# Kernel optimization log

Hardware: AMD Instinct MI355X
Metric: run time of the kernel (lower is better)

Reference implementation:

```python
import jax, jax.numpy as jnp
import numpy as np

B, N, E = 4, 8192, 65536
OBS, H, OUT, NOUT = 128, 256, 1024, 18


def setup_inputs() -> dict:
    key = jax.random.key(0)
    ks = jax.random.split(key, 8)
    nodes = jax.random.normal(ks[0], (B, N, OBS), dtype=jnp.float32)
    edges = jax.random.randint(ks[1], (B, 2, E), 0, N, dtype=jnp.int64)
    # Glorot-ish init for weights
    W0 = jax.random.normal(ks[2], (OBS, H), dtype=jnp.float32) / np.float32(np.sqrt(OBS))
    W1 = jax.random.normal(ks[3], (H, OUT), dtype=jnp.float32) / np.float32(np.sqrt(H))
    W_logit = jax.random.normal(ks[4], (OUT, NOUT), dtype=jnp.float32) / np.float32(np.sqrt(OUT))
    W_val = jax.random.normal(ks[5], (OUT, 1), dtype=jnp.float32) / np.float32(np.sqrt(OUT))
    return {
        "nodes": nodes, "edges": edges,
        "W0": W0, "b0": jnp.zeros((H,), jnp.float32),
        "W1": W1, "b1": jnp.zeros((OUT,), jnp.float32),
        "W_logit": W_logit, "b_logit": jnp.zeros((NOUT,), jnp.float32),
        "W_val": W_val, "b_val": jnp.zeros((1,), jnp.float32),
    }


def _gcn_layer(x, src, dst, W, b, n):
    # PyG GCNConv: out = D^{-1/2} (A + I) D^{-1/2} X W + b   (self-loops already in src/dst)
    h = x @ W                                                     # [N, F_out]
    deg = jax.ops.segment_sum(jnp.ones(src.shape, jnp.float32), dst, num_segments=n)
    dinv = jnp.where(deg > 0, jax.lax.rsqrt(deg), 0.0)            # deg^{-1/2}
    norm = dinv[src] * dinv[dst]                                  # [Etot]
    msg = h[src] * norm[:, None]                                  # gather + normalize
    agg = jax.ops.segment_sum(msg, dst, num_segments=n)           # scatter-add
    return agg + b


def reference(nodes, edges, W0, b0, W1, b1, W_logit, b_logit, W_val, b_val):
    n = nodes.shape[1]
    loops = jnp.arange(n, dtype=edges.dtype)  # self-loops, added by GCNConv

    def per_graph(x, ei):
        src = jnp.concatenate([ei[0], loops])
        dst = jnp.concatenate([ei[1], loops])
        h = jax.nn.relu(_gcn_layer(x, src, dst, W0, b0, n))
        # (original applies F.dropout here; omitted for a deterministic reference)
        h = jax.nn.relu(_gcn_layer(h, src, dst, W1, b1, n))
        return h

    out = jax.vmap(per_graph)(nodes, edges)        # [B, N, OUT]
    logits = out @ W_logit + b_logit               # [B, N, NOUT]
    values = (out @ W_val + b_val)[..., 0]         # [B, N]
    return logits, values
```

## Files before the change

kernel.cpp:

```cpp
#include <hip/hip_runtime.h>
#include <hip/hip_bf16.h>

#define BB   4
#define NN   8192
#define EE   65536
#define FOBS 128
#define FH   256
#define FOUT 1024
#define NLOG 18
#define P20  20
#define BKT  64

typedef __attribute__((ext_vector_type(8))) short frag8;
typedef __attribute__((ext_vector_type(4))) float f32x4;

__device__ __forceinline__ ushort f2b(float v) {
    __hip_bfloat16 h = __float2bfloat16(v);
    return *reinterpret_cast<ushort*>(&h);
}
__device__ __forceinline__ float blo(uint u) { return __uint_as_float(u << 16); }
__device__ __forceinline__ float bhi(uint u) { return __uint_as_float(u & 0xffff0000u); }


#define W0_N   (FOBS * FH)
#define W1_N   (FH * FOUT)
#define WH_N   (19 * FOUT)
#define CUR_N  (BB * NN)
#define PREP_TOTAL (W0_N + W1_N + WH_N + CUR_N)

__global__ void prep_kernel(const float* __restrict__ W0, ushort* __restrict__ W0T,
                            const float* __restrict__ W1, ushort* __restrict__ W1T,
                            const float* __restrict__ Wl, const float* __restrict__ Wv,
                            ushort* __restrict__ WT19, int* __restrict__ cursor) {
    int idx = blockIdx.x * blockDim.x + threadIdx.x;
    if (idx < W0_N) {
        int n = idx / FOBS, k = idx - n * FOBS;
        W0T[idx] = f2b(W0[(size_t)k * FH + n]);
        return;
    }
    idx -= W0_N;
    if (idx < W1_N) {
        int n = idx / FH, k = idx - n * FH;
        W1T[idx] = f2b(W1[(size_t)k * FOUT + n]);
        return;
    }
    idx -= W1_N;
    if (idx < WH_N) {
        int o = idx >> 10, k = idx & (FOUT - 1);
        WT19[idx] = f2b((o < NLOG) ? Wl[(size_t)k * NLOG + o] : Wv[k]);
        return;
    }
    idx -= WH_N;
    if (idx < CUR_N) cursor[idx] = 0;
}

__global__ void bucket_fill(const int* __restrict__ edges, int* __restrict__ cursor,
                            int* __restrict__ bucket) {
    int blk = blockIdx.x;
    int xcd = blk & 7;
    int g = xcd >> 1;
    int chunk = (blk >> 3) * 2 + (xcd & 1);
    int e = chunk * 256 + threadIdx.x;
    const int* src = edges + (size_t)g * 2 * EE;
    const int* dst = src + EE;
    int d = dst[e];
    int slot = atomicAdd(&cursor[(size_t)g * NN + d], 1);
    if (slot < BKT) bucket[((size_t)g * NN + d) * BKT + slot] = src[e];
}

__global__ __launch_bounds__(256) void gather_agg_f32(
    const float* __restrict__ x_all, const int* __restrict__ cnt_all,
    const int* __restrict__ bucket, uint* __restrict__ agg_all)
{
    int blk = blockIdx.x;
    int xcd = blk & 7;
    int g = xcd >> 1;
    int local = (blk >> 3) * 2 + (xcd & 1);
    int wv = threadIdx.x >> 6, lane = threadIdx.x & 63;
    int n = local * 4 + wv;

    const float2* x = (const float2*)(x_all + (size_t)g * NN * FOBS);
    const int* cnt = cnt_all + (size_t)g * NN;
    const int* bkt = bucket + ((size_t)g * NN + n) * BKT;

    int cn = cnt[n];
    float wn = rsqrtf((float)cn + 1.0f);
    int deg = min(cn, BKT);

    float2 self = x[(size_t)n * 64 + lane];
    float ax = wn * wn * self.x, ay = wn * wn * self.y;

    for (int i = 0; i < deg; i += 8) {
        int last = deg - 1;
        int s0 = bkt[i];
        int s1 = bkt[min(i + 1, last)], s2 = bkt[min(i + 2, last)], s3 = bkt[min(i + 3, last)];
        int s4 = bkt[min(i + 4, last)], s5 = bkt[min(i + 5, last)], s6 = bkt[min(i + 6, last)];
        int s7 = bkt[min(i + 7, last)];
        float w0 = rsqrtf((float)cnt[s0] + 1.0f) * wn;
        float w1 = (i + 1 < deg) ? rsqrtf((float)cnt[s1] + 1.0f) * wn : 0.0f;
        float w2 = (i + 2 < deg) ? rsqrtf((float)cnt[s2] + 1.0f) * wn : 0.0f;
        float w3 = (i + 3 < deg) ? rsqrtf((float)cnt[s3] + 1.0f) * wn : 0.0f;
        float w4 = (i + 4 < deg) ? rsqrtf((float)cnt[s4] + 1.0f) * wn : 0.0f;
        float w5 = (i + 5 < deg) ? rsqrtf((float)cnt[s5] + 1.0f) * wn : 0.0f;
        float w6 = (i + 6 < deg) ? rsqrtf((float)cnt[s6] + 1.0f) * wn : 0.0f;
        float w7 = (i + 7 < deg) ? rsqrtf((float)cnt[s7] + 1.0f) * wn : 0.0f;
        float2 r0 = x[(size_t)s0 * 64 + lane], r1 = x[(size_t)s1 * 64 + lane];
        float2 r2 = x[(size_t)s2 * 64 + lane], r3 = x[(size_t)s3 * 64 + lane];
        float2 r4 = x[(size_t)s4 * 64 + lane], r5 = x[(size_t)s5 * 64 + lane];
        float2 r6 = x[(size_t)s6 * 64 + lane], r7 = x[(size_t)s7 * 64 + lane];
        ax += w0 * r0.x + w1 * r1.x + w2 * r2.x + w3 * r3.x
            + w4 * r4.x + w5 * r5.x + w6 * r6.x + w7 * r7.x;
        ay += w0 * r0.y + w1 * r1.y + w2 * r2.y + w3 * r3.y
            + w4 * r4.y + w5 * r5.y + w6 * r6.y + w7 * r7.y;
    }
    agg_all[((size_t)g * NN + n) * 64 + lane] = (uint)f2b(ax) | ((uint)f2b(ay) << 16);
}

__global__ __launch_bounds__(256) void gather_agg_b256(
    const uint2* __restrict__ xb_all, const int* __restrict__ cnt_all,
    const int* __restrict__ bucket, uint2* __restrict__ agg_all)
{
    int blk = blockIdx.x;
    int xcd = blk & 7;
    int g = xcd >> 1;
    int local = (blk >> 3) * 2 + (xcd & 1);
    int wv = threadIdx.x >> 6, lane = threadIdx.x & 63;
    int n = local * 4 + wv;

    const uint2* xb = xb_all + (size_t)g * NN * 64;
    const int* cnt = cnt_all + (size_t)g * NN;
    const int* bkt = bucket + ((size_t)g * NN + n) * BKT;

    int cn = cnt[n];
    float wn = rsqrtf((float)cn + 1.0f);
    int deg = min(cn, BKT);

    uint2 u = xb[(size_t)n * 64 + lane];
    float w2s = wn * wn;
    float a0 = w2s * blo(u.x), a1 = w2s * bhi(u.x), a2 = w2s * blo(u.y), a3 = w2s * bhi(u.y);

    for (int i = 0; i < deg; i += 8) {
        int last = deg - 1;
        int s0 = bkt[i];
        int s1 = bkt[min(i + 1, last)], s2 = bkt[min(i + 2, last)], s3 = bkt[min(i + 3, last)];
        int s4 = bkt[min(i + 4, last)], s5 = bkt[min(i + 5, last)], s6 = bkt[min(i + 6, last)];
        int s7 = bkt[min(i + 7, last)];
        float w0 = rsqrtf((float)cnt[s0] + 1.0f) * wn;
        float w1 = (i + 1 < deg) ? rsqrtf((float)cnt[s1] + 1.0f) * wn : 0.0f;
        float w2 = (i + 2 < deg) ? rsqrtf((float)cnt[s2] + 1.0f) * wn : 0.0f;
        float w3 = (i + 3 < deg) ? rsqrtf((float)cnt[s3] + 1.0f) * wn : 0.0f;
        float w4 = (i + 4 < deg) ? rsqrtf((float)cnt[s4] + 1.0f) * wn : 0.0f;
        float w5 = (i + 5 < deg) ? rsqrtf((float)cnt[s5] + 1.0f) * wn : 0.0f;
        float w6 = (i + 6 < deg) ? rsqrtf((float)cnt[s6] + 1.0f) * wn : 0.0f;
        float w7 = (i + 7 < deg) ? rsqrtf((float)cnt[s7] + 1.0f) * wn : 0.0f;
        uint2 r0 = xb[(size_t)s0 * 64 + lane], r1 = xb[(size_t)s1 * 64 + lane];
        uint2 r2 = xb[(size_t)s2 * 64 + lane], r3 = xb[(size_t)s3 * 64 + lane];
        uint2 r4 = xb[(size_t)s4 * 64 + lane], r5 = xb[(size_t)s5 * 64 + lane];
        uint2 r6 = xb[(size_t)s6 * 64 + lane], r7 = xb[(size_t)s7 * 64 + lane];
        a0 += w0 * blo(r0.x) + w1 * blo(r1.x) + w2 * blo(r2.x) + w3 * blo(r3.x)
            + w4 * blo(r4.x) + w5 * blo(r5.x) + w6 * blo(r6.x) + w7 * blo(r7.x);
        a1 += w0 * bhi(r0.x) + w1 * bhi(r1.x) + w2 * bhi(r2.x) + w3 * bhi(r3.x)
            + w4 * bhi(r4.x) + w5 * bhi(r5.x) + w6 * bhi(r6.x) + w7 * bhi(r7.x);
        a2 += w0 * blo(r0.y) + w1 * blo(r1.y) + w2 * blo(r2.y) + w3 * blo(r3.y)
            + w4 * blo(r4.y) + w5 * blo(r5.y) + w6 * blo(r6.y) + w7 * blo(r7.y);
        a3 += w0 * bhi(r0.y) + w1 * bhi(r1.y) + w2 * bhi(r2.y) + w3 * bhi(r3.y)
            + w4 * bhi(r4.y) + w5 * bhi(r5.y) + w6 * bhi(r6.y) + w7 * bhi(r7.y);
    }
    uint2 o;
    o.x = (uint)f2b(a0) | ((uint)f2b(a1) << 16);
    o.y = (uint)f2b(a2) | ((uint)f2b(a3) << 16);
    agg_all[((size_t)g * NN + n) * 64 + lane] = o;
}

__global__ __launch_bounds__(256) void mfma_gemm(
    const ushort* __restrict__ A_all, const ushort* __restrict__ BT,
    const float* __restrict__ bias, ushort* __restrict__ C_all,
    int M, int N, int K, int relu)
{
    __shared__ ushort As[128][72];
    __shared__ ushort Bs[128][72];

    int blk = blockIdx.x;
    int xcd = blk & 7;
    int g = xcd >> 1;
    int tid = (blk >> 3) * 2 + (xcd & 1);
    int bn = tid & 1, bm = tid >> 1;

    const ushort* A = A_all + (size_t)g * M * K;
    ushort* C = C_all + (size_t)g * M * N;

    int t = threadIdx.x;
    int lane = t & 63, w = t >> 6;
    int wm = w >> 1, wn = w & 1;
    int l15 = lane & 15, quad = lane >> 4;

    f32x4 acc[4][4] = {};

    int srow = t >> 3, scol = (t & 7) * 8;
    const ushort* Abase = A + (size_t)(bm * 128) * K;
    const ushort* Bbase = BT + (size_t)(bn * 128) * K;

    for (int k0 = 0; k0 < K; k0 += 64) {
#pragma unroll
        for (int i = 0; i < 4; ++i) {
            int row = srow + 32 * i;
            *(uint4*)&As[row][scol] = *(const uint4*)(Abase + (size_t)row * K + k0 + scol);
        }
#pragma unroll
        for (int i = 0; i < 4; ++i) {
            int row = srow + 32 * i;
            *(uint4*)&Bs[row][scol] = *(const uint4*)(Bbase + (size_t)row * K + k0 + scol);
        }
        __syncthreads();
#pragma unroll
        for (int kk = 0; kk < 64; kk += 32) {
            frag8 af[4], bf[4];
#pragma unroll
            for (int i = 0; i < 4; ++i)
                af[i] = *(const frag8*)&As[wm * 64 + i * 16 + l15][kk + quad * 8];
#pragma unroll
            for (int j = 0; j < 4; ++j)
                bf[j] = *(const frag8*)&Bs[wn * 64 + j * 16 + l15][kk + quad * 8];
#pragma unroll
            for (int i = 0; i < 4; ++i)
#pragma unroll
                for (int j = 0; j < 4; ++j)
                    acc[i][j] = __builtin_amdgcn_mfma_f32_16x16x32_bf16(af[i], bf[j], acc[i][j], 0, 0, 0);
        }
        __syncthreads();
    }

#pragma unroll
    for (int i = 0; i < 4; ++i) {
#pragma unroll
        for (int j = 0; j < 4; ++j) {
            int col = bn * 128 + wn * 64 + j * 16 + l15;
            float bcol = bias[col];
#pragma unroll
            for (int r = 0; r < 4; ++r) {
                int row = bm * 128 + wm * 64 + i * 16 + quad * 4 + r;
                float v = acc[i][j][r] + bcol;
                if (relu) v = fmaxf(v, 0.0f);
                C[(size_t)row * N + col] = f2b(v);
            }
        }
    }
}

__global__ __launch_bounds__(256) void gemm2_heads(
    const ushort* __restrict__ hagg_all,
    const ushort* __restrict__ W1T,
    const float*  __restrict__ b1,
    const ushort* __restrict__ WT19,
    float* __restrict__ partial)
{
    __shared__ __align__(16) ushort smem[2 * 128 * 72];
    __shared__ __align__(16) ushort wt[20][136];

    ushort* As = smem;
    ushort* Bs = smem + 128 * 72;
    ushort* Ct = smem;

    int blk = blockIdx.x;
    int xcd = blk & 7;
    int g = xcd >> 1;
    int tid = (blk >> 3) * 2 + (xcd & 1);
    int sp = tid & 1, bm = tid >> 1;

    int t = threadIdx.x;
    int lane = t & 63, w = t >> 6;
    int wm = w >> 1, wn = w & 1;
    int l15 = lane & 15, quad = lane >> 4;
    int srow = t >> 3, scol = (t & 7) * 8;

    const ushort* A0 = hagg_all + ((size_t)g * NN + bm * 128) * FH;

    if (t < 136) wt[19][t] = 0;

    f32x4 hacc[2][2] = {};

    for (int bi = 0; bi < 4; ++bi) {
        int bn = sp * 4 + bi;
        __syncthreads();

        for (int idx = t; idx < 19 * 16; idx += 256) {
            int row = idx >> 4, c8 = (idx & 15) * 8;
            *(uint4*)&wt[row][c8] = *(const uint4*)(WT19 + (size_t)row * FOUT + bn * 128 + c8);
        }

        f32x4 acc[4][4] = {};
        const ushort* Bbase = W1T + (size_t)(bn * 128) * FH;

        for (int k0 = 0; k0 < FH; k0 += 64) {
#pragma unroll
            for (int i = 0; i < 4; ++i) {
                int row = srow + 32 * i;
                *(uint4*)&As[row * 72 + scol] = *(const uint4*)(A0 + (size_t)row * FH + k0 + scol);
                *(uint4*)&Bs[row * 72 + scol] = *(const uint4*)(Bbase + (size_t)row * FH + k0 + scol);
            }
            __syncthreads();
#pragma unroll
            for (int kk = 0; kk < 64; kk += 32) {
                frag8 af[4], bf[4];
#pragma unroll
                for (int i = 0; i < 4; ++i)
                    af[i] = *(const frag8*)&As[(wm * 64 + i * 16 + l15) * 72 + kk + quad * 8];
#pragma unroll
                for (int j = 0; j < 4; ++j)
                    bf[j] = *(const frag8*)&Bs[(wn * 64 + j * 16 + l15) * 72 + kk + quad * 8];
#pragma unroll
                for (int i = 0; i < 4; ++i)
#pragma unroll
                    for (int j = 0; j < 4; ++j)
                        acc[i][j] = __builtin_amdgcn_mfma_f32_16x16x32_bf16(af[i], bf[j], acc[i][j], 0, 0, 0);
            }
            __syncthreads();
        }

#pragma unroll
        for (int j = 0; j < 4; ++j) {
            int colL = wn * 64 + j * 16 + l15;
            float bcol = b1[bn * 128 + colL];
#pragma unroll
            for (int i = 0; i < 4; ++i) {
                int rowL = wm * 64 + i * 16 + quad * 4;
#pragma unroll
                for (int r = 0; r < 4; ++r) {
                    float v = fmaxf(acc[i][j][r] + bcol, 0.0f);
                    Ct[(size_t)(rowL + r) * 136 + colL] = f2b(v);
                }
            }
        }
        __syncthreads();

        int r1 = (l15 < 3) ? (16 + l15) : 19;
#pragma unroll
        for (int kk = 0; kk < 128; kk += 32) {
            frag8 b0 = *(const frag8*)&wt[l15][kk + quad * 8];
            frag8 bO = *(const frag8*)&wt[r1][kk + quad * 8];
#pragma unroll
            for (int mt = 0; mt < 2; ++mt) {
                int row = (w * 2 + mt) * 16 + l15;
                frag8 af = *(const frag8*)&Ct[(size_t)row * 136 + kk + quad * 8];
                hacc[mt][0] = __builtin_amdgcn_mfma_f32_16x16x32_bf16(af, b0, hacc[mt][0], 0, 0, 0);
                hacc[mt][1] = __builtin_amdgcn_mfma_f32_16x16x32_bf16(af, bO, hacc[mt][1], 0, 0, 0);
            }
        }
    }

#pragma unroll
    for (int mt = 0; mt < 2; ++mt) {
#pragma unroll
        for (int r = 0; r < 4; ++r) {
            int node = bm * 128 + (w * 2 + mt) * 16 + quad * 4 + r;
            size_t base = ((size_t)(sp * BB + g) * NN + node) * P20;
            partial[base + l15] = hacc[mt][0][r];
            if (l15 < 3) partial[base + 16 + l15] = hacc[mt][1][r];
        }
    }
}

__global__ void heads_combine(const float* __restrict__ partial,
                              const float* __restrict__ bl, const float* __restrict__ bv,
                              float* __restrict__ out_logits, float* __restrict__ out_values) {
    int i = blockIdx.x * blockDim.x + threadIdx.x;
    if (i >= BB * NN * 19) return;
    int o = i % 19;
    int gn = i / 19;
    float v = partial[(size_t)gn * P20 + o] + partial[((size_t)BB * NN + gn) * P20 + o];
    if (o < NLOG) out_logits[(size_t)gn * NLOG + o] = v + bl[o];
    else          out_values[gn] = v + bv[0];
}

extern "C" void kernel_launch(void* const* d_in, const int* in_sizes, int n_in,
                              void* d_out, int out_size, void* d_ws, size_t ws_size,
                              hipStream_t stream) {
    const float* nodes = (const float*)d_in[0];
    const int*   edges = (const int*)d_in[1];
    const float* W0 = (const float*)d_in[2];
    const float* b0 = (const float*)d_in[3];
    const float* W1 = (const float*)d_in[4];
    const float* b1 = (const float*)d_in[5];
    const float* Wl = (const float*)d_in[6];
    const float* bl = (const float*)d_in[7];
    const float* Wv = (const float*)d_in[8];
    const float* bv = (const float*)d_in[9];

    float* out_logits = (float*)d_out;
    float* out_values = out_logits + (size_t)BB * NN * NLOG;

    char* ws = (char*)d_ws;
    int*    cursor  = (int*)(ws);
    ushort* W0T     = (ushort*)(ws + (128 << 10));
    ushort* W1T     = (ushort*)(ws + (192 << 10));
    ushort* WT19    = (ushort*)(ws + (704 << 10));
    int*    bucket  = (int*)(ws + (1u << 20));
    ushort* xagg_b  = (ushort*)(ws + (9u << 20));
    ushort* h1b     = (ushort*)(ws + (17u << 20));
    ushort* hagg_b  = (ushort*)(ws + (33u << 20));
    float*  partial = (float*)(ws + (49u << 20));

    prep_kernel<<<(PREP_TOTAL + 255) / 256, 256, 0, stream>>>(
        W0, W0T, W1, W1T, Wl, Wv, WT19, cursor);

    bucket_fill<<<1024, 256, 0, stream>>>(edges, cursor, bucket);

    gather_agg_f32<<<8192, 256, 0, stream>>>(nodes, cursor, bucket, (uint*)xagg_b);

    mfma_gemm<<<512, 256, 0, stream>>>(xagg_b, W0T, b0, h1b, NN, FH, FOBS, 1);

    gather_agg_b256<<<8192, 256, 0, stream>>>((const uint2*)h1b, cursor, bucket,
                                              (uint2*)hagg_b);

    gemm2_heads<<<512, 256, 0, stream>>>(hagg_b, W1T, b1, WT19, partial);

    heads_combine<<<(BB * NN * 19 + 255) / 256, 256, 0, stream>>>(partial, bl, bv,
                                                                  out_logits, out_values);
}
```

Before: 195.7 us.

## Restructure fused GEMM2+heads: full-K resident A tile, double-buffered W1, drop combine kernel

Rewrites the second GEMM fused with the output heads so each block owns a 128-row tile across all 1024 output columns. The full-K A tile stays resident in LDS and W1/head-weight tiles are register-prefetched into a double buffer, so the next tile loads while the current one computes. Because a block no longer splits the column range, the heads accumulate fully in registers and are written directly with biases. This removes the partial buffer and the separate combine kernel. The trade-off is only 256 blocks, each using about 156 KB of dynamic LDS, which lowers occupancy and parallelism on a 256-CU device.

```diff
diff --git a/kernel.cpp b/kernel.cpp
--- a/kernel.cpp
+++ b/kernel.cpp
@@ -8,7 +8,6 @@
 #define FH   256
 #define FOUT 1024
 #define NLOG 18
-#define P20  20
 #define BKT  64
 
 typedef __attribute__((ext_vector_type(8))) short frag8;
@@ -20,7 +19,6 @@
 }
 __device__ __forceinline__ float blo(uint u) { return __uint_as_float(u << 16); }
 __device__ __forceinline__ float bhi(uint u) { return __uint_as_float(u & 0xffff0000u); }
-
 
 #define W0_N   (FOBS * FH)
 #define W1_N   (FH * FOUT)
@@ -247,129 +245,150 @@
     }
 }
 
-__global__ __launch_bounds__(256) void gemm2_heads(
+#define LDS_AS   0
+#define LDS_BS   33792
+#define LDS_BSZ  16896
+#define LDS_CT   67584
+#define LDS_WT   76800
+#define LDS_WTSZ 1440
+#define LDS_SHORTS 79680
+
+__global__ __launch_bounds__(256) void gemm2_heads_v2(
     const ushort* __restrict__ hagg_all,
     const ushort* __restrict__ W1T,
     const float*  __restrict__ b1,
     const ushort* __restrict__ WT19,
-    float* __restrict__ partial)
+    const float* __restrict__ bl, const float* __restrict__ bv,
+    float* __restrict__ out_logits_all, float* __restrict__ out_values_all)
 {
-    __shared__ __align__(16) ushort smem[2 * 128 * 72];
-    __shared__ __align__(16) ushort wt[20][136];
-
-    ushort* As = smem;
-    ushort* Bs = smem + 128 * 72;
-    ushort* Ct = smem;
+    extern __shared__ __align__(16) ushort smem[];
 
     int blk = blockIdx.x;
-    int xcd = blk & 7;
-    int g = xcd >> 1;
-    int tid = (blk >> 3) * 2 + (xcd & 1);
-    int sp = tid & 1, bm = tid >> 1;
-
+    int g = blk & 3, bm = blk >> 2;
     int t = threadIdx.x;
     int lane = t & 63, w = t >> 6;
-    int wm = w >> 1, wn = w & 1;
     int l15 = lane & 15, quad = lane >> 4;
-    int srow = t >> 3, scol = (t & 7) * 8;
 
     const ushort* A0 = hagg_all + ((size_t)g * NN + bm * 128) * FH;
 
-    if (t < 136) wt[19][t] = 0;
+#pragma unroll
+    for (int c = 0; c < 16; ++c) {
+        int idx = c * 256 + t;
+        int row = idx >> 5, c8 = (idx & 31) * 8;
+        *(uint4*)&smem[LDS_AS + row * 264 + c8] = *(const uint4*)(A0 + (size_t)row * FH + c8);
+    }
+#pragma unroll
+    for (int c = 0; c < 8; ++c) {
+        int idx = c * 256 + t;
+        int row = idx >> 5, c8 = (idx & 31) * 8;
+        *(uint4*)&smem[LDS_BS + row * 264 + c8] = *(const uint4*)(W1T + (size_t)row * FH + c8);
+    }
+    if (t < 152) {
+        int row = t >> 3, c8 = (t & 7) * 8;
+        *(uint4*)&smem[LDS_WT + row * 72 + c8] = *(const uint4*)(WT19 + (size_t)row * FOUT + c8);
+    }
+    if (t < 16) {
+        int b = t >> 3, c8 = (t & 7) * 8;
+        uint4 z = {0, 0, 0, 0};
+        *(uint4*)&smem[LDS_WT + b * LDS_WTSZ + 19 * 72 + c8] = z;
+    }
+    __syncthreads();
 
     f32x4 hacc[2][2] = {};
-
-    for (int bi = 0; bi < 4; ++bi) {
-        int bn = sp * 4 + bi;
+    int r1 = (l15 < 3) ? (16 + l15) : 19;
+
+    for (int bn = 0; bn < 16; ++bn) {
+        int cur = bn & 1, nxt = cur ^ 1;
+
+        uint4 pb[8];
+        uint4 pw;
+        if (bn < 15) {
+            const ushort* Bn = W1T + (size_t)(bn + 1) * 64 * FH;
+#pragma unroll
+            for (int c = 0; c < 8; ++c) {
+                int idx = c * 256 + t;
+                int row = idx >> 5, c8 = (idx & 31) * 8;
+                pb[c] = *(const uint4*)(Bn + (size_t)row * FH + c8);
+            }
+            if (t < 152) {
+                int row = t >> 3, c8 = (t & 7) * 8;
+                pw = *(const uint4*)(WT19 + (size_t)row * FOUT + (bn + 1) * 64 + c8);
+            }
+        }
+
+        const ushort* Bb  = &smem[LDS_BS + cur * LDS_BSZ];
+        const ushort* wtb = &smem[LDS_WT + cur * LDS_WTSZ];
+
+        f32x4 acc[2][4] = {};
+#pragma unroll
+        for (int kk = 0; kk < 256; kk += 32) {
+            frag8 af[2], bf[4];
+#pragma unroll
+            for (int mt = 0; mt < 2; ++mt)
+                af[mt] = *(const frag8*)&smem[LDS_AS + (w * 32 + mt * 16 + l15) * 264 + kk + quad * 8];
+#pragma unroll
+            for (int nt = 0; nt < 4; ++nt)
+                bf[nt] = *(const frag8*)&Bb[(nt * 16 + l15) * 264 + kk + quad * 8];
+#pragma unroll
+            for (int mt = 0; mt < 2; ++mt)
+#pragma unroll
+                for (int nt = 0; nt < 4; ++nt)
+                    acc[mt][nt] = __builtin_amdgcn_mfma_f32_16x16x32_bf16(af[mt], bf[nt], acc[mt][nt], 0, 0, 0);
+        }
+
+#pragma unroll
+        for (int nt = 0; nt < 4; ++nt) {
+            float bcol = b1[bn * 64 + nt * 16 + l15];
+#pragma unroll
+            for (int mt = 0; mt < 2; ++mt) {
+                int rbase = w * 32 + mt * 16 + quad * 4;
+#pragma unroll
+                for (int r = 0; r < 4; ++r) {
+                    float v = fmaxf(acc[mt][nt][r] + bcol, 0.0f);
+                    smem[LDS_CT + (rbase + r) * 72 + nt * 16 + l15] = f2b(v);
+                }
+            }
+        }
+
+#pragma unroll
+        for (int kk2 = 0; kk2 < 64; kk2 += 32) {
+            frag8 hb0 = *(const frag8*)&wtb[l15 * 72 + kk2 + quad * 8];
+            frag8 hb1 = *(const frag8*)&wtb[r1 * 72 + kk2 + quad * 8];
+#pragma unroll
+            for (int mt = 0; mt < 2; ++mt) {
+                frag8 haf = *(const frag8*)&smem[LDS_CT + (w * 32 + mt * 16 + l15) * 72 + kk2 + quad * 8];
+                hacc[mt][0] = __builtin_amdgcn_mfma_f32_16x16x32_bf16(haf, hb0, hacc[mt][0], 0, 0, 0);
+                hacc[mt][1] = __builtin_amdgcn_mfma_f32_16x16x32_bf16(haf, hb1, hacc[mt][1], 0, 0, 0);
+            }
+        }
+
+        if (bn < 15) {
+#pragma unroll
+            for (int c = 0; c < 8; ++c) {
+                int idx = c * 256 + t;
+                int row = idx >> 5, c8 = (idx & 31) * 8;
+                *(uint4*)&smem[LDS_BS + nxt * LDS_BSZ + row * 264 + c8] = pb[c];
+            }
+            if (t < 152) {
+                int row = t >> 3, c8 = (t & 7) * 8;
+                *(uint4*)&smem[LDS_WT + nxt * LDS_WTSZ + row * 72 + c8] = pw;
+            }
+        }
         __syncthreads();
-
-        for (int idx = t; idx < 19 * 16; idx += 256) {
-            int row = idx >> 4, c8 = (idx & 15) * 8;
-            *(uint4*)&wt[row][c8] = *(const uint4*)(WT19 + (size_t)row * FOUT + bn * 128 + c8);
-        }
-
-        f32x4 acc[4][4] = {};
-        const ushort* Bbase = W1T + (size_t)(bn * 128) * FH;
-
-        for (int k0 = 0; k0 < FH; k0 += 64) {
-#pragma unroll
-            for (int i = 0; i < 4; ++i) {
-                int row = srow + 32 * i;
-                *(uint4*)&As[row * 72 + scol] = *(const uint4*)(A0 + (size_t)row * FH + k0 + scol);
-                *(uint4*)&Bs[row * 72 + scol] = *(const uint4*)(Bbase + (size_t)row * FH + k0 + scol);
-            }
-            __syncthreads();
-#pragma unroll
-            for (int kk = 0; kk < 64; kk += 32) {
-                frag8 af[4], bf[4];
-#pragma unroll
-                for (int i = 0; i < 4; ++i)
-                    af[i] = *(const frag8*)&As[(wm * 64 + i * 16 + l15) * 72 + kk + quad * 8];
-#pragma unroll
-                for (int j = 0; j < 4; ++j)
-                    bf[j] = *(const frag8*)&Bs[(wn * 64 + j * 16 + l15) * 72 + kk + quad * 8];
-#pragma unroll
-                for (int i = 0; i < 4; ++i)
-#pragma unroll
-                    for (int j = 0; j < 4; ++j)
-                        acc[i][j] = __builtin_amdgcn_mfma_f32_16x16x32_bf16(af[i], bf[j], acc[i][j], 0, 0, 0);
-            }
-            __syncthreads();
-        }
-
-#pragma unroll
-        for (int j = 0; j < 4; ++j) {
-            int colL = wn * 64 + j * 16 + l15;
-            float bcol = b1[bn * 128 + colL];
-#pragma unroll
-            for (int i = 0; i < 4; ++i) {
-                int rowL = wm * 64 + i * 16 + quad * 4;
-#pragma unroll
-                for (int r = 0; r < 4; ++r) {
-                    float v = fmaxf(acc[i][j][r] + bcol, 0.0f);
-                    Ct[(size_t)(rowL + r) * 136 + colL] = f2b(v);
-                }
-            }
-        }
-        __syncthreads();
-
-        int r1 = (l15 < 3) ? (16 + l15) : 19;
-#pragma unroll
-        for (int kk = 0; kk < 128; kk += 32) {
-            frag8 b0 = *(const frag8*)&wt[l15][kk + quad * 8];
-            frag8 bO = *(const frag8*)&wt[r1][kk + quad * 8];
-#pragma unroll
-            for (int mt = 0; mt < 2; ++mt) {
-                int row = (w * 2 + mt) * 16 + l15;
-                frag8 af = *(const frag8*)&Ct[(size_t)row * 136 + kk + quad * 8];
-                hacc[mt][0] = __builtin_amdgcn_mfma_f32_16x16x32_bf16(af, b0, hacc[mt][0], 0, 0, 0);
-                hacc[mt][1] = __builtin_amdgcn_mfma_f32_16x16x32_bf16(af, bO, hacc[mt][1], 0, 0, 0);
-            }
-        }
-    }
-
+    }
+
+    float* out_logits = out_logits_all + (size_t)g * NN * NLOG;
+    float* out_values = out_values_all + (size_t)g * NN;
 #pragma unroll
     for (int mt = 0; mt < 2; ++mt) {
 #pragma unroll
         for (int r = 0; r < 4; ++r) {
-            int node = bm * 128 + (w * 2 + mt) * 16 + quad * 4 + r;
-            size_t base = ((size_t)(sp * BB + g) * NN + node) * P20;
-            partial[base + l15] = hacc[mt][0][r];
-            if (l15 < 3) partial[base + 16 + l15] = hacc[mt][1][r];
-        }
-    }
-}
-
-__global__ void heads_combine(const float* __restrict__ partial,
-                              const float* __restrict__ bl, const float* __restrict__ bv,
-                              float* __restrict__ out_logits, float* __restrict__ out_values) {
-    int i = blockIdx.x * blockDim.x + threadIdx.x;
-    if (i >= BB * NN * 19) return;
-    int o = i % 19;
-    int gn = i / 19;
-    float v = partial[(size_t)gn * P20 + o] + partial[((size_t)BB * NN + gn) * P20 + o];
-    if (o < NLOG) out_logits[(size_t)gn * NLOG + o] = v + bl[o];
-    else          out_values[gn] = v + bv[0];
+            int node = bm * 128 + w * 32 + mt * 16 + quad * 4 + r;
+            out_logits[(size_t)node * NLOG + l15] = hacc[mt][0][r] + bl[l15];
+            if (l15 < 2)       out_logits[(size_t)node * NLOG + 16 + l15] = hacc[mt][1][r] + bl[16 + l15];
+            else if (l15 == 2) out_values[node] = hacc[mt][1][r] + bv[0];
+        }
+    }
 }
 
 extern "C" void kernel_launch(void* const* d_in, const int* in_sizes, int n_in,
@@ -398,7 +417,10 @@
     ushort* xagg_b  = (ushort*)(ws + (9u << 20));
     ushort* h1b     = (ushort*)(ws + (17u << 20));
     ushort* hagg_b  = (ushort*)(ws + (33u << 20));
-    float*  partial = (float*)(ws + (49u << 20));
+
+    hipFuncSetAttribute((const void*)gemm2_heads_v2,
+                        hipFuncAttributeMaxDynamicSharedMemorySize,
+                        LDS_SHORTS * 2);
 
     prep_kernel<<<(PREP_TOTAL + 255) / 256, 256, 0, stream>>>(
         W0, W0T, W1, W1T, Wl, Wv, WT19, cursor);
@@ -412,8 +434,6 @@
     gather_agg_b256<<<8192, 256, 0, stream>>>((const uint2*)h1b, cursor, bucket,
                                               (uint2*)hagg_b);
 
-    gemm2_heads<<<512, 256, 0, stream>>>(hagg_b, W1T, b1, WT19, partial);
-
-    heads_combine<<<(BB * NN * 19 + 255) / 256, 256, 0, stream>>>(partial, bl, bv,
-                                                                  out_logits, out_values);
-}
+    gemm2_heads_v2<<<256, 256, LDS_SHORTS * 2, stream>>>(
+        hagg_b, W1T, b1, WT19, bl, bv, out_logits, out_values);
+}
```

After: 241.5 us. 23.4% more time.
